# Optimization experiments

Hardware: AMD Instinct MI355X
Metric: run time of the kernel (lower is better)

Reference implementation:

```python
import jax, jax.numpy as jnp
from jax import lax
import numpy as np

B, H, W = 8, 256, 256
BIG = 1e4  # sentinel distance, > H + W; BIG**2 safe in fp32
EPS = 1e-8
# loss weights (LossConfig defaults)
W_DICE, W_TVERSKY, W_BOUNDARY, W_ATTN = 1.0, 0.7, 0.5, 0.3
ALPHA, BETA = 0.3, 0.7


def _edt2d(mask):
    """Exact 2D Euclidean distance to nearest True pixel. mask: [H, W] bool.
    Separable: 1D column distance via scans, then per-row lower envelope
    min_{x'} g[y,x']^2 + (x-x')^2 done by a vectorized brute-force min."""
    Hh, Ww = mask.shape
    yy = jnp.arange(Hh, dtype=jnp.float32)[:, None]                      # [H,1]
    up = lax.associative_scan(jnp.maximum, jnp.where(mask, yy, -BIG), axis=0)
    dn = lax.associative_scan(jnp.minimum, jnp.where(mask, yy, 2.0 * BIG), axis=0, reverse=True)
    g = jnp.minimum(jnp.minimum(yy - up, dn - yy), BIG)                  # [H,W] column distance
    xs = jnp.arange(Ww, dtype=jnp.float32)
    delta2 = (xs[:, None] - xs[None, :]) ** 2                            # [W,W']
    d2 = jnp.min(g[:, None, :] ** 2 + delta2[None, :, :], axis=-1)       # [H,W]
    return jnp.sqrt(d2)


def _abs_sdt(mask):
    # |neg - pos| where pos/neg are zero on complementary regions => pos + neg
    any_fg = jnp.any(mask)
    a = _edt2d(mask) + _edt2d(~mask)
    return jnp.where(any_fg, a, jnp.zeros_like(a))


def setup_inputs() -> dict:
    key = jax.random.key(0)
    k1, k2, k3 = jax.random.split(key, 3)
    probs = jax.random.uniform(k1, (B, 1, H, W), dtype=jnp.float32)
    targets = jax.random.randint(k2, (B, 1, H, W), 0, 2, dtype=jnp.int32)
    attention_map = jax.random.uniform(k3, (B, 1, H, W), dtype=jnp.float32)
    return {"probs": probs, "targets": targets, "attention_map": attention_map}


def reference(probs, targets, attention_map):
    t = targets.astype(jnp.float32)
    p2 = probs.reshape(probs.shape[0], -1)
    t2 = t.reshape(t.shape[0], -1)

    # dice
    inter = jnp.sum(p2 * t2, axis=1)
    union = jnp.sum(p2, axis=1) + jnp.sum(t2, axis=1)
    dl = 1.0 - jnp.mean((2.0 * inter + EPS) / (union + EPS))

    # tversky
    tp = inter
    fn = jnp.sum(t2 * (1.0 - p2), axis=1)
    fp = jnp.sum((1.0 - t2) * p2, axis=1)
    tl = 1.0 - jnp.mean((tp + EPS) / (tp + ALPHA * fn + BETA * fp + EPS))

    # boundary: per-sample mean of probs * |SDT(target)|, averaged over batch
    masks = t[:, 0] > 0.5                                               # [B,H,W]
    sdt_abs = jax.vmap(_abs_sdt)(masks)                                  # [B,H,W]
    bl = jnp.mean(probs[:, 0] * sdt_abs)

    # attention consistency (MSE)
    al = jnp.mean((attention_map - t) ** 2)

    total = W_DICE * dl + W_TVERSKY * tl + W_BOUNDARY * bl + W_ATTN * al
    return total
```

## Files before the change

kernel.cpp:

```cpp
#include <hip/hip_runtime.h>

#define HW_ELEMS 65536
#define BIGD 1e4f
#define EPSL 1e-8f
#define NBLK 2048

__device__ __forceinline__ float waveSum(float v) {
  #pragma unroll
  for (int off = 32; off > 0; off >>= 1) v += __shfl_down(v, off);
  return v;
}

__global__ __launch_bounds__(256) void fused_kernel(
    const float* __restrict__ probs, const int* __restrict__ targets,
    const float* __restrict__ attn, float* __restrict__ partial) {
  const int blk = blockIdx.x;
  const int b = blk >> 8;
  const int y = blk & 255;
  const int x = threadIdx.x;
  const int* __restrict__ timg = targets + b * HW_ELEMS;

  const int rowoff = b * HW_ELEMS + y * 256 + x;
  const float p = probs[rowoff];
  const float a = attn[rowoff];
  const int t0 = timg[y * 256 + x];
  const float tf = (float)t0;

  float dpos = t0 ? 0.f : BIGD;
  float dneg = t0 ? BIGD : 0.f;
  for (int r = 1; r < 256; r += 4) {
    if (dpos < BIGD && dneg < BIGD) break;
    int tu[4], td[4];
    #pragma unroll
    for (int j = 0; j < 4; ++j) {
      const int yu = y - (r + j), yd = y + (r + j);
      tu[j] = (yu >= 0)  ? timg[yu * 256 + x] : -1;
      td[j] = (yd < 256) ? timg[yd * 256 + x] : -1;
    }
    #pragma unroll
    for (int j = 0; j < 4; ++j) {
      const float fr = (float)(r + j);
      if (tu[j] == 1) dpos = fminf(dpos, fr); else if (tu[j] == 0) dneg = fminf(dneg, fr);
      if (td[j] == 1) dpos = fminf(dpos, fr); else if (td[j] == 0) dneg = fminf(dneg, fr);
    }
  }

  __shared__ float g2p[256], g2n[256];
  g2p[x] = dpos * dpos;
  g2n[x] = dneg * dneg;
  __syncthreads();

  float m2p = g2p[x], m2n = g2n[x];
  for (int r = 1; r < 256; r += 4) {
    const float rr0 = (float)(r * r);
    if (rr0 >= m2p && rr0 >= m2n) break;
    #pragma unroll
    for (int j = 0; j < 4; ++j) {
      const int rj = r + j;
      const float rr = (float)(rj * rj);
      const int xl = x - rj, xr = x + rj;
      if (xl >= 0)  { m2p = fminf(m2p, rr + g2p[xl]); m2n = fminf(m2n, rr + g2n[xl]); }
      if (xr < 256) { m2p = fminf(m2p, rr + g2p[xr]); m2n = fminf(m2n, rr + g2n[xr]); }
    }
  }

  const float sdt = sqrtf(m2p) + sqrtf(m2n);
  const float contrib = p * sdt;
  const float d = a - tf;

  const float v0 = waveSum(p * tf);
  const float v1 = waveSum(p);
  const float v2 = waveSum(tf);
  const float v3 = waveSum(d * d);
  const float v4 = waveSum(contrib);

  __shared__ float lds[4][5];
  const int wid = threadIdx.x >> 6, lane = threadIdx.x & 63;
  if (lane == 0) {
    lds[wid][0] = v0; lds[wid][1] = v1; lds[wid][2] = v2;
    lds[wid][3] = v3; lds[wid][4] = v4;
  }
  __syncthreads();
  if (threadIdx.x == 0) {
    float s[5] = {0.f, 0.f, 0.f, 0.f, 0.f};
    #pragma unroll
    for (int w = 0; w < 4; ++w)
      #pragma unroll
      for (int q = 0; q < 5; ++q) s[q] += lds[w][q];
    #pragma unroll
    for (int q = 0; q < 5; ++q) partial[q * NBLK + blk] = s[q];
  }
}

__global__ __launch_bounds__(256) void finalize_kernel(
    const float* __restrict__ partial, float* __restrict__ out) {
  const int tid = threadIdx.x;
  __shared__ float red[32][8];
  __shared__ float sred[4];

  const int pair = tid >> 3, sub = tid & 7;
  const int qsel = pair >> 3;
  const int bb = pair & 7;
  const int qoff[4] = {0, 1, 2, 4};
  const int base = qoff[qsel] * NBLK + bb * 256 + sub * 32;
  float s = 0.f;
  #pragma unroll
  for (int j = 0; j < 32; ++j) s += partial[base + j];
  red[pair][sub] = s;

  float e = 0.f;
  #pragma unroll
  for (int j = 0; j < 8; ++j) e += partial[3 * NBLK + tid * 8 + j];
  e = waveSum(e);
  if ((tid & 63) == 0) sred[tid >> 6] = e;
  __syncthreads();

  if (tid == 0) {
    float dsum = 0.f, tsum = 0.f, bsum = 0.f;
    for (int b2 = 0; b2 < 8; ++b2) {
      float inter = 0.f, sp = 0.f, st = 0.f, bd = 0.f;
      #pragma unroll
      for (int k = 0; k < 8; ++k) {
        inter += red[0 * 8 + b2][k];
        sp    += red[1 * 8 + b2][k];
        st    += red[2 * 8 + b2][k];
        bd    += red[3 * 8 + b2][k];
      }
      dsum += (2.f * inter + EPSL) / (sp + st + EPSL);
      const float fn = st - inter;
      const float fp = sp - inter;
      tsum += (inter + EPSL) / (inter + 0.3f * fn + 0.7f * fp + EPSL);
      bsum += (st > 0.5f) ? bd : 0.f;
    }
    const float sse = sred[0] + sred[1] + sred[2] + sred[3];
    const float dl = 1.f - dsum * 0.125f;
    const float tl = 1.f - tsum * 0.125f;
    const float bl = bsum * (1.f / 524288.f);
    const float al = sse * (1.f / 524288.f);
    out[0] = 1.0f * dl + 0.7f * tl + 0.5f * bl + 0.3f * al;
  }
}

extern "C" void kernel_launch(void* const* d_in, const int* in_sizes, int n_in,
                              void* d_out, int out_size, void* d_ws, size_t ws_size,
                              hipStream_t stream) {
  const float* probs   = (const float*)d_in[0];
  const int*   targets = (const int*)d_in[1];
  const float* attn    = (const float*)d_in[2];
  float* out = (float*)d_out;
  float* partial = (float*)d_ws;
  fused_kernel<<<NBLK, 256, 0, stream>>>(probs, targets, attn, partial);
  finalize_kernel<<<1, 256, 0, stream>>>(partial, out);
}
```

Baseline: 71.49 us.

## Process two rows per block and share a preloaded column window of targets

Each block now handles two adjacent rows. It loads an 18-row window of target values into registers once, which serves the vertical distance search for both rows, and falls back to per-row global loads only beyond radius 8. The horizontal envelope loop unrolls the first 8 radii without an early-exit check and then continues with a per-radius break. The grid is halved and the finalize kernel indexing is adjusted to match. This trades fewer blocks and some redundant window loads for less repeated target traffic and loop overhead, with added register pressure.

```diff
diff --git a/kernel.cpp b/kernel.cpp
--- a/kernel.cpp
+++ b/kernel.cpp
@@ -3,7 +3,7 @@
 #define HW_ELEMS 65536
 #define BIGD 1e4f
 #define EPSL 1e-8f
-#define NBLK 2048
+#define NBLK 1024
 
 __device__ __forceinline__ float waveSum(float v) {
   #pragma unroll
@@ -15,64 +15,90 @@
     const float* __restrict__ probs, const int* __restrict__ targets,
     const float* __restrict__ attn, float* __restrict__ partial) {
   const int blk = blockIdx.x;
-  const int b = blk >> 8;
-  const int y = blk & 255;
+  const int b = blk >> 7;
+  const int y0 = (blk & 127) * 2;
   const int x = threadIdx.x;
   const int* __restrict__ timg = targets + b * HW_ELEMS;
 
-  const int rowoff = b * HW_ELEMS + y * 256 + x;
-  const float p = probs[rowoff];
-  const float a = attn[rowoff];
-  const int t0 = timg[y * 256 + x];
-  const float tf = (float)t0;
+  const int base = b * HW_ELEMS + y0 * 256 + x;
+  const float p0 = probs[base], p1 = probs[base + 256];
+  const float a0 = attn[base],  a1 = attn[base + 256];
 
-  float dpos = t0 ? 0.f : BIGD;
-  float dneg = t0 ? BIGD : 0.f;
-  for (int r = 1; r < 256; r += 4) {
-    if (dpos < BIGD && dneg < BIGD) break;
-    int tu[4], td[4];
+  int w[18];
+  #pragma unroll
+  for (int j = 0; j < 18; ++j) {
+    const int yy = y0 - 8 + j;
+    w[j] = (yy >= 0 && yy < 256) ? timg[yy * 256 + x] : -1;
+  }
+  const float tf0 = (w[8] == 1) ? 1.f : 0.f;
+  const float tf1 = (w[9] == 1) ? 1.f : 0.f;
+
+  float dpos[2] = {BIGD, BIGD}, dneg[2] = {BIGD, BIGD};
+  #pragma unroll
+  for (int k = 0; k < 2; ++k) {
+    const int c = 8 + k;
     #pragma unroll
-    for (int j = 0; j < 4; ++j) {
-      const int yu = y - (r + j), yd = y + (r + j);
-      tu[j] = (yu >= 0)  ? timg[yu * 256 + x] : -1;
-      td[j] = (yd < 256) ? timg[yd * 256 + x] : -1;
+    for (int j = 0; j < 18; ++j) {
+      const float dy = fabsf((float)(j - c));
+      if (w[j] == 1) dpos[k] = fminf(dpos[k], dy);
+      else if (w[j] == 0) dneg[k] = fminf(dneg[k], dy);
     }
-    #pragma unroll
-    for (int j = 0; j < 4; ++j) {
-      const float fr = (float)(r + j);
-      if (tu[j] == 1) dpos = fminf(dpos, fr); else if (tu[j] == 0) dneg = fminf(dneg, fr);
-      if (td[j] == 1) dpos = fminf(dpos, fr); else if (td[j] == 0) dneg = fminf(dneg, fr);
+  }
+  #pragma unroll
+  for (int k = 0; k < 2; ++k) {
+    const int yk = y0 + k;
+    for (int r = 9; r < 256; ++r) {
+      const float fr = (float)r;
+      if (dpos[k] < fr && dneg[k] < fr) break;
+      const int yu = yk - r, yd = yk + r;
+      if (yu >= 0) {
+        if (timg[yu * 256 + x]) dpos[k] = fminf(dpos[k], fr);
+        else                    dneg[k] = fminf(dneg[k], fr);
+      }
+      if (yd < 256) {
+        if (timg[yd * 256 + x]) dpos[k] = fminf(dpos[k], fr);
+        else                    dneg[k] = fminf(dneg[k], fr);
+      }
     }
   }
 
-  __shared__ float g2p[256], g2n[256];
-  g2p[x] = dpos * dpos;
-  g2n[x] = dneg * dneg;
+  __shared__ float g2p[2][256], g2n[2][256];
+  g2p[0][x] = dpos[0] * dpos[0];
+  g2n[0][x] = dneg[0] * dneg[0];
+  g2p[1][x] = dpos[1] * dpos[1];
+  g2n[1][x] = dneg[1] * dneg[1];
   __syncthreads();
 
-  float m2p = g2p[x], m2n = g2n[x];
-  for (int r = 1; r < 256; r += 4) {
-    const float rr0 = (float)(r * r);
-    if (rr0 >= m2p && rr0 >= m2n) break;
+  float m2p[2], m2n[2];
+  #pragma unroll
+  for (int k = 0; k < 2; ++k) {
+    m2p[k] = g2p[k][x];
+    m2n[k] = g2n[k][x];
     #pragma unroll
-    for (int j = 0; j < 4; ++j) {
-      const int rj = r + j;
-      const float rr = (float)(rj * rj);
-      const int xl = x - rj, xr = x + rj;
-      if (xl >= 0)  { m2p = fminf(m2p, rr + g2p[xl]); m2n = fminf(m2n, rr + g2n[xl]); }
-      if (xr < 256) { m2p = fminf(m2p, rr + g2p[xr]); m2n = fminf(m2n, rr + g2n[xr]); }
+    for (int j = 1; j <= 8; ++j) {
+      const float rr = (float)(j * j);
+      const int xl = x - j, xr = x + j;
+      if (xl >= 0)  { m2p[k] = fminf(m2p[k], rr + g2p[k][xl]); m2n[k] = fminf(m2n[k], rr + g2n[k][xl]); }
+      if (xr < 256) { m2p[k] = fminf(m2p[k], rr + g2p[k][xr]); m2n[k] = fminf(m2n[k], rr + g2n[k][xr]); }
+    }
+    for (int r = 9; r < 256; ++r) {
+      const float rr0 = (float)(r * r);
+      if (rr0 >= m2p[k] && rr0 >= m2n[k]) break;
+      const int xl = x - r, xr = x + r;
+      if (xl >= 0)  { m2p[k] = fminf(m2p[k], rr0 + g2p[k][xl]); m2n[k] = fminf(m2n[k], rr0 + g2n[k][xl]); }
+      if (xr < 256) { m2p[k] = fminf(m2p[k], rr0 + g2p[k][xr]); m2n[k] = fminf(m2n[k], rr0 + g2n[k][xr]); }
     }
   }
 
-  const float sdt = sqrtf(m2p) + sqrtf(m2n);
-  const float contrib = p * sdt;
-  const float d = a - tf;
+  const float sdt0 = sqrtf(m2p[0]) + sqrtf(m2n[0]);
+  const float sdt1 = sqrtf(m2p[1]) + sqrtf(m2n[1]);
+  const float d0 = a0 - tf0, d1 = a1 - tf1;
 
-  const float v0 = waveSum(p * tf);
-  const float v1 = waveSum(p);
-  const float v2 = waveSum(tf);
-  const float v3 = waveSum(d * d);
-  const float v4 = waveSum(contrib);
+  const float v0 = waveSum(p0 * tf0 + p1 * tf1);
+  const float v1 = waveSum(p0 + p1);
+  const float v2 = waveSum(tf0 + tf1);
+  const float v3 = waveSum(d0 * d0 + d1 * d1);
+  const float v4 = waveSum(p0 * sdt0 + p1 * sdt1);
 
   __shared__ float lds[4][5];
   const int wid = threadIdx.x >> 6, lane = threadIdx.x & 63;
@@ -84,9 +110,9 @@
   if (threadIdx.x == 0) {
     float s[5] = {0.f, 0.f, 0.f, 0.f, 0.f};
     #pragma unroll
-    for (int w = 0; w < 4; ++w)
+    for (int w2 = 0; w2 < 4; ++w2)
       #pragma unroll
-      for (int q = 0; q < 5; ++q) s[q] += lds[w][q];
+      for (int q = 0; q < 5; ++q) s[q] += lds[w2][q];
     #pragma unroll
     for (int q = 0; q < 5; ++q) partial[q * NBLK + blk] = s[q];
   }
@@ -102,15 +128,15 @@
   const int qsel = pair >> 3;
   const int bb = pair & 7;
   const int qoff[4] = {0, 1, 2, 4};
-  const int base = qoff[qsel] * NBLK + bb * 256 + sub * 32;
+  const int base = qoff[qsel] * NBLK + bb * 128 + sub * 16;
   float s = 0.f;
   #pragma unroll
-  for (int j = 0; j < 32; ++j) s += partial[base + j];
+  for (int j = 0; j < 16; ++j) s += partial[base + j];
   red[pair][sub] = s;
 
   float e = 0.f;
   #pragma unroll
-  for (int j = 0; j < 8; ++j) e += partial[3 * NBLK + tid * 8 + j];
+  for (int j = 0; j < 4; ++j) e += partial[3 * NBLK + tid * 4 + j];
   e = waveSum(e);
   if ((tid & 63) == 0) sred[tid >> 6] = e;
   __syncthreads();
```

Result: slower. 74.83 us (+4.7%).
